# Optimization experiments

Hardware: AMD Instinct MI355X
Metric: run time of the kernel (lower is better)

## Reference

```python
import jax, jax.numpy as jnp
import numpy as np

N = 100_000      # nodes
E = 1_600_000    # edges (before self-loops)
IN_DIM = 128
HID = 64
NEG_SLOPE = 0.2  # PyG GATConv default


def gat_layer(x, src, dst, W, att_src, att_dst, bias, heads, out_ch):
    """PyG-style GATConv: messages flow src -> dst, softmax over incoming edges of dst."""
    n = x.shape[0]
    h = (x @ W).reshape(n, heads, out_ch)                 # [N,H,C]
    a_src = jnp.einsum('nhc,hc->nh', h, att_src)          # [N,H]
    a_dst = jnp.einsum('nhc,hc->nh', h, att_dst)          # [N,H]
    e = jax.nn.leaky_relu(a_src[src] + a_dst[dst], NEG_SLOPE)  # [E,H]
    # segment softmax over edges grouped by destination node
    m = jax.ops.segment_max(e, dst, num_segments=n)       # [N,H]
    ex = jnp.exp(e - m[dst])                              # [E,H]
    denom = jax.ops.segment_sum(ex, dst, num_segments=n)  # [N,H]
    alpha = ex / denom[dst]                               # [E,H]
    msg = alpha[:, :, None] * h[src]                      # [E,H,C]
    out = jax.ops.segment_sum(msg, dst, num_segments=n)   # [N,H,C]
    return out.reshape(n, heads * out_ch) + bias


def setup_inputs() -> dict:
    key = jax.random.key(0)
    ks = jax.random.split(key, 12)
    s = 0.1
    x = jax.random.normal(ks[0], (N, IN_DIM), jnp.float32)
    edge_index = jax.random.randint(ks[1], (2, E), 0, N, dtype=jnp.int32)
    # conv1: in_dim -> hidden, heads=2 (concat)
    W1 = jax.random.normal(ks[2], (IN_DIM, 2 * HID), jnp.float32) * s
    att_src1 = jax.random.normal(ks[3], (2, HID), jnp.float32) * s
    att_dst1 = jax.random.normal(ks[4], (2, HID), jnp.float32) * s
    b1 = jnp.zeros((2 * HID,), jnp.float32)
    # conv2: 2*hidden -> 1, heads=1
    W2 = jax.random.normal(ks[5], (2 * HID, 1), jnp.float32) * s
    att_src2 = jax.random.normal(ks[6], (1, 1), jnp.float32) * s
    att_dst2 = jax.random.normal(ks[7], (1, 1), jnp.float32) * s
    b2 = jnp.zeros((1,), jnp.float32)
    return {"x": x, "edge_index": edge_index,
            "W1": W1, "att_src1": att_src1, "att_dst1": att_dst1, "b1": b1,
            "W2": W2, "att_src2": att_src2, "att_dst2": att_dst2, "b2": b2}


def reference(x, edge_index, W1, att_src1, att_dst1, b1, W2, att_src2, att_dst2, b2):
    n = x.shape[0]
    # PyG GATConv default: add self-loops
    loop = jnp.arange(n, dtype=edge_index.dtype)
    src = jnp.concatenate([edge_index[0], loop])
    dst = jnp.concatenate([edge_index[1], loop])
    h = jax.nn.relu(gat_layer(x, src, dst, W1, att_src1, att_dst1, b1, heads=2, out_ch=HID))
    out = gat_layer(h, src, dst, W2, att_src2, att_dst2, b2, heads=1, out_ch=1)
    return jax.nn.sigmoid(out)  # [N,1]
```

## Files before the change

### kernel.cpp

```cpp
#include <hip/hip_runtime.h>
#include <hip/hip_bf16.h>
#include <hip/hip_fp8.h>
#include <hip/hip_fp16.h>

#define NEG 0.2f
#define CAP 48
#define TILE 8192
typedef unsigned int u32;
typedef unsigned short u16;
typedef unsigned char u8;
typedef unsigned long long u64;
typedef __attribute__((ext_vector_type(8))) short s8v;
typedef __attribute__((ext_vector_type(4))) float f4v;
typedef __attribute__((ext_vector_type(2))) float f2v;

__global__ __launch_bounds__(256) void binA_k(const int* __restrict__ ei,
                                              int2* __restrict__ meta,
                                              u64* __restrict__ slabs,
                                              int E, int Etot, int NB, int ntiles){
  __shared__ int bcnt[512], sc[512], bcur[512];
  int tile = blockIdx.x, tid = threadIdx.x;
  int base = tile*TILE;
  int cnt = min(TILE, Etot - base);
  for (int i=tid;i<512;i+=256) bcnt[i]=0;
  __syncthreads();
  for (int i=tid;i<cnt;i+=256){
    int e = base+i;
    int d = (e<E)? ei[E+e] : e-E;
    atomicAdd(&bcnt[d>>8], 1);
  }
  __syncthreads();
  for (int i=tid;i<512;i+=256) sc[i]=bcnt[i];
  __syncthreads();
  for (int o=1;o<512;o<<=1){
    int i0=tid, i1=tid+256;
    int r0 = (i0>=o)? sc[i0-o]:0;
    int r1 = (i1>=o)? sc[i1-o]:0;
    __syncthreads();
    sc[i0]+=r0; sc[i1]+=r1;
    __syncthreads();
  }
  for (int i=tid;i<512;i+=256) bcur[i] = sc[i]-bcnt[i];
  __syncthreads();
  for (int b=tid;b<NB;b+=256)
    meta[(size_t)b*ntiles + tile] = make_int2(sc[b]-bcnt[b], bcnt[b]);
  for (int i=tid;i<cnt;i+=256){
    int e = base+i;
    int d = (e<E)? ei[E+e] : e-E;
    int s = (e<E)? ei[e]   : d;
    int p = atomicAdd(&bcur[d>>8], 1);
    slabs[(size_t)base + p] = ((u64)(u32)d << 32) | (u32)s;
  }
}

__global__ __launch_bounds__(256) void binB_k(const u64* __restrict__ slabs,
                                              const int2* __restrict__ meta,
                                              const float2* __restrict__ as1,
                                              const float2* __restrict__ ad1,
                                              int* __restrict__ cur,
                                              u64* __restrict__ combo,
                                              float2* __restrict__ den,
                                              int N, int ntiles){
  int b = blockIdx.x, tid = threadIdx.x;
  int lo = b<<8;
  int nn = min(256, N-lo);
  __shared__ int lcur[256];
  __shared__ float sden0[256], sden1[256];
  __shared__ float2 sad[256];
  lcur[tid]=0; sden0[tid]=0.f; sden1[tid]=0.f;
  sad[tid] = (tid<nn)? ad1[lo+tid] : make_float2(0.f,0.f);
  __syncthreads();
  int grp = tid>>4, l16 = tid&15;
  const int2* mrow = meta + (size_t)b*ntiles;
  for (int t=grp; t<ntiles; t+=16){
    int2 m = mrow[t];
    const u64* sp = slabs + (size_t)t*TILE + m.x;
    for (int i=l16; i<m.y; i+=16){
      u64 pk = sp[i];
      int d = (int)(pk>>32), s = (int)(u32)pk;
      int dl = d & 255;
      float2 av = as1[s];
      float2 adv = sad[dl];
      float e0 = av.x+adv.x; e0 = (e0>0.f)? e0 : NEG*e0;
      float e1 = av.y+adv.y; e1 = (e1>0.f)? e1 : NEG*e1;
      __half2 hw = __floats2half2_rn(__expf(e0), __expf(e1));
      float2 wr = __half22float2(hw);
      atomicAdd(&sden0[dl], wr.x);
      atomicAdd(&sden1[dl], wr.y);
      int p = atomicAdd(&lcur[dl], 1);
      u32 wb = *(u32*)&hw;
      if (p < CAP) combo[(size_t)p*N + d] = ((u64)wb << 32) | (u32)s;
    }
  }
  __syncthreads();
  if (tid < nn){
    cur[lo+tid] = lcur[tid];
    den[lo+tid] = make_float2(sden0[tid], sden1[tid]);
  }
}

__global__ __launch_bounds__(256) void wt_k(const float* __restrict__ W, u16* __restrict__ Wt){
  int g = blockIdx.x*256 + threadIdx.x;
  int k = g >> 7, c = g & 127;
  __hip_bfloat16 b = __float2bfloat16(W[g]);
  Wt[c*128 + k] = *(u16*)&b;
}

__global__ __launch_bounds__(256) void gemm_k(const float* __restrict__ x,
                                              const u16* __restrict__ Wt,
                                              const float* __restrict__ aw_s,
                                              const float* __restrict__ aw_d,
                                              u8*  __restrict__ h1f,
                                              float2* __restrict__ as1,
                                              float2* __restrict__ ad1, int N){
  __shared__ u16 xs[128*136];
  __shared__ u16 ws[128*136];
  int tid = threadIdx.x;
  int rowBase = blockIdx.x * 128;
  #pragma unroll
  for (int i=0;i<16;i++){
    int j = i*256 + tid;
    int c = j >> 5, k4 = j & 31;
    *(uint2*)&ws[c*136 + k4*4] = ((const uint2*)Wt)[j];
  }
  #pragma unroll
  for (int i=0;i<16;i++){
    int j = i*256 + tid;
    int r = j >> 5, c4 = j & 31;
    float4 v = make_float4(0.f,0.f,0.f,0.f);
    if (rowBase + r < N) v = ((const float4*)x)[(size_t)(rowBase+r)*32 + c4];
    __hip_bfloat16 b0=__float2bfloat16(v.x), b1=__float2bfloat16(v.y);
    __hip_bfloat16 b2=__float2bfloat16(v.z), b3=__float2bfloat16(v.w);
    u32 w0 = (u32)*(u16*)&b0 | ((u32)*(u16*)&b1 << 16);
    u32 w1 = (u32)*(u16*)&b2 | ((u32)*(u16*)&b3 << 16);
    *(uint2*)&xs[r*136 + c4*4] = make_uint2(w0, w1);
  }
  __syncthreads();
  int wv = tid >> 6, lane = tid & 63;
  int lr = lane & 15, lk = lane >> 4;
  f4v acc[2][8];
  #pragma unroll
  for (int rt=0;rt<2;rt++)
    #pragma unroll
    for (int ct=0;ct<8;ct++) acc[rt][ct] = (f4v){0.f,0.f,0.f,0.f};
  #pragma unroll
  for (int ks=0; ks<4; ks++){
    int koff = ks*32 + lk*8;
    s8v bfrag[8];
    #pragma unroll
    for (int ct=0; ct<8; ct++)
      bfrag[ct] = *(s8v*)&ws[(ct*16 + lr)*136 + koff];
    #pragma unroll
    for (int rt=0; rt<2; rt++){
      int row = wv*32 + rt*16 + lr;
      s8v afrag = *(s8v*)&xs[row*136 + koff];
      #pragma unroll
      for (int ct=0; ct<8; ct++)
        acc[rt][ct] = __builtin_amdgcn_mfma_f32_16x16x32_bf16(afrag, bfrag[ct], acc[rt][ct], 0,0,0);
    }
  }
  #pragma unroll
  for (int rt=0; rt<2; rt++){
    float lps0[4]={0,0,0,0}, lps1[4]={0,0,0,0}, lpd0[4]={0,0,0,0}, lpd1[4]={0,0,0,0};
    int nodeB = rowBase + wv*32 + rt*16 + lk*4;
    #pragma unroll
    for (int ct=0; ct<8; ct++){
      int ch = ct*16 + lr;
      float aws = aw_s[ch], awd = aw_d[ch];
      #pragma unroll
      for (int reg=0; reg<4; reg++){
        float v = acc[rt][ct][reg];
        if (ct < 4){ lps0[reg] = fmaf(v, aws, lps0[reg]); lpd0[reg] = fmaf(v, awd, lpd0[reg]); }
        else       { lps1[reg] = fmaf(v, aws, lps1[reg]); lpd1[reg] = fmaf(v, awd, lpd1[reg]); }
      }
      int pk01 = __builtin_amdgcn_cvt_pk_fp8_f32(acc[rt][ct][0], acc[rt][ct][1], 0, false);
      int pk23 = __builtin_amdgcn_cvt_pk_fp8_f32(acc[rt][ct][2], acc[rt][ct][3], 0, false);
      if (nodeB + 0 < N) h1f[(size_t)(nodeB+0)*128 + ch] = (u8)(pk01 & 0xff);
      if (nodeB + 1 < N) h1f[(size_t)(nodeB+1)*128 + ch] = (u8)((pk01 >> 8) & 0xff);
      if (nodeB + 2 < N) h1f[(size_t)(nodeB+2)*128 + ch] = (u8)(pk23 & 0xff);
      if (nodeB + 3 < N) h1f[(size_t)(nodeB+3)*128 + ch] = (u8)((pk23 >> 8) & 0xff);
    }
    #pragma unroll
    for (int reg=0; reg<4; reg++){
      float a=lps0[reg], b=lps1[reg], c=lpd0[reg], d=lpd1[reg];
      #pragma unroll
      for (int o=1;o<16;o<<=1){
        a += __shfl_xor(a,o); b += __shfl_xor(b,o);
        c += __shfl_xor(c,o); d += __shfl_xor(d,o);
      }
      int node = nodeB + reg;
      if (lr == 0 && node < N){
        as1[node] = make_float2(a, b);
        ad1[node] = make_float2(c, d);
      }
    }
  }
}

__global__ __launch_bounds__(256) void agg1_k(const uint2* __restrict__ h1f2,
                                              const u64* __restrict__ combo,
                                              const float2* __restrict__ den,
                                              const int* __restrict__ cur,
                                              const float4* __restrict__ b1_4,
                                              const float4* __restrict__ W2_4,
                                              float* __restrict__ h2, int N){
  int w = threadIdx.x >> 6, l = threadIdx.x & 63;
  int g = l >> 4, li = l & 15;
  int n = blockIdx.x*16 + w*4 + g;
  if (n >= N) return;
  int deg = min(cur[n], CAP);
  bool hsel = (li >= 8);
  float2 dn = den[n];
  float rd = 1.f / (hsel ? dn.y : dn.x);
  float ac0=0.f,ac1=0.f,ac2=0.f,ac3=0.f,ac4=0.f,ac5=0.f,ac6=0.f,ac7=0.f;
  for (int kk = 0; kk < deg; kk += 8){
    u64 pk[8]; bool vd[8];
    #pragma unroll
    for (int j=0;j<8;j++){
      int idx = kk + j;
      vd[j] = idx < deg;
      pk[j] = combo[(size_t)(vd[j] ? idx : 0)*N + n];
    }
    uint2 hv[8];
    #pragma unroll
    for (int j=0;j<8;j++) hv[j] = h1f2[(size_t)(u32)(pk[j] & 0xffffffffu)*16 + li];
    #pragma unroll
    for (int j=0;j<8;j++){
      u32 wb = (u32)(pk[j] >> 32);
      __half2 hw = *(__half2*)&wb;
      float2 wf = __half22float2(hw);
      float gw = hsel ? wf.y : wf.x;
      gw = vd[j] ? gw : 0.f;
      f2v p0 = __builtin_amdgcn_cvt_pk_f32_fp8((int)hv[j].x, false);
      f2v p1 = __builtin_amdgcn_cvt_pk_f32_fp8((int)hv[j].x, true);
      f2v p2 = __builtin_amdgcn_cvt_pk_f32_fp8((int)hv[j].y, false);
      f2v p3 = __builtin_amdgcn_cvt_pk_f32_fp8((int)hv[j].y, true);
      ac0 = fmaf(gw, p0.x, ac0); ac1 = fmaf(gw, p0.y, ac1);
      ac2 = fmaf(gw, p1.x, ac2); ac3 = fmaf(gw, p1.y, ac3);
      ac4 = fmaf(gw, p2.x, ac4); ac5 = fmaf(gw, p2.y, ac5);
      ac6 = fmaf(gw, p3.x, ac6); ac7 = fmaf(gw, p3.y, ac7);
    }
  }
  float4 bb0 = b1_4[li*2], bb1 = b1_4[li*2+1];
  float4 ww0 = W2_4[li*2], ww1 = W2_4[li*2+1];
  float p = 0.f;
  p = fmaf(fmaxf(fmaf(ac0, rd, bb0.x), 0.f), ww0.x, p);
  p = fmaf(fmaxf(fmaf(ac1, rd, bb0.y), 0.f), ww0.y, p);
  p = fmaf(fmaxf(fmaf(ac2, rd, bb0.z), 0.f), ww0.z, p);
  p = fmaf(fmaxf(fmaf(ac3, rd, bb0.w), 0.f), ww0.w, p);
  p = fmaf(fmaxf(fmaf(ac4, rd, bb1.x), 0.f), ww1.x, p);
  p = fmaf(fmaxf(fmaf(ac5, rd, bb1.y), 0.f), ww1.y, p);
  p = fmaf(fmaxf(fmaf(ac6, rd, bb1.z), 0.f), ww1.z, p);
  p = fmaf(fmaxf(fmaf(ac7, rd, bb1.w), 0.f), ww1.w, p);
  #pragma unroll
  for (int o=1;o<16;o<<=1) p += __shfl_xor(p,o);
  if (li == 0) h2[n] = p;
}

__global__ __launch_bounds__(256) void agg2_k(const float* __restrict__ h2,
                                              const int* __restrict__ cur,
                                              const u64* __restrict__ combo,
                                              const float* __restrict__ att_s2,
                                              const float* __restrict__ att_d2,
                                              const float* __restrict__ b2,
                                              float* __restrict__ out, int N){
  int w = threadIdx.x >> 6, l = threadIdx.x & 63;
  int n = blockIdx.x*4 + w;
  if (n >= N) return;
  float as2 = att_s2[0], ad2 = att_d2[0];
  float hd = h2[n]*ad2;
  int deg = min(cur[n], CAP);
  bool v = l < deg;
  int s = (int)(u32)(combo[(size_t)(v ? l : 0)*N + n] & 0xffffffffu);
  float hs = h2[s];
  float e = fmaf(hs, as2, hd); e = (e>0.f)? e : NEG*e;
  float xv = v ? __expf(e) : 0.f;
  float den = xv, wsum = xv*hs;
  #pragma unroll
  for (int o=32;o>0;o>>=1){ den += __shfl_xor(den,o); wsum += __shfl_xor(wsum,o); }
  if (l == 0){
    float z = wsum/den + b2[0];
    out[n] = 1.f/(1.f + __expf(-z));
  }
}

extern "C" void kernel_launch(void* const* d_in, const int* in_sizes, int n_in,
                              void* d_out, int out_size, void* d_ws, size_t ws_size,
                              hipStream_t stream){
  const float* x     = (const float*)d_in[0];
  const int*   ei    = (const int*)d_in[1];
  const float* W1    = (const float*)d_in[2];
  const float* aw_s  = (const float*)d_in[3];
  const float* aw_d  = (const float*)d_in[4];
  const float* b1    = (const float*)d_in[5];
  const float* W2    = (const float*)d_in[6];
  const float* at_s2 = (const float*)d_in[7];
  const float* at_d2 = (const float*)d_in[8];
  const float* b2    = (const float*)d_in[9];
  float* out = (float*)d_out;

  const int N = in_sizes[0]/128;
  const int E = in_sizes[1]/2;
  const int Etot = E + N;
  const int ntiles = (Etot + TILE - 1) / TILE;
  const int NB = (N + 255) >> 8;

  auto align256 = [](size_t v){ return (v + 255) & ~(size_t)255; };
  char* w = (char*)d_ws;
  u8* h1f       = (u8*)w;     w += align256((size_t)N*128);
  float2* as1   = (float2*)w; w += align256((size_t)N*8);
  float2* ad1   = (float2*)w; w += align256((size_t)N*8);
  float* h2     = (float*)w;  w += align256((size_t)N*4);
  int* cur      = (int*)w;    w += align256((size_t)N*4);
  float2* den   = (float2*)w; w += align256((size_t)N*8);
  u16* Wt       = (u16*)w;    w += align256((size_t)128*128*2);
  u64* combo    = (u64*)w;    w += align256((size_t)N*CAP*8);
  u64* slabs    = (u64*)w;    w += align256((size_t)ntiles*TILE*8);
  int2* meta    = (int2*)w;   w += align256((size_t)NB*ntiles*8);

  const int tb = 256;
  binA_k<<<ntiles, tb, 0, stream>>>(ei, meta, slabs, E, Etot, NB, ntiles);
  wt_k<<<64, tb, 0, stream>>>(W1, Wt);
  gemm_k<<<(N+127)/128, tb, 0, stream>>>(x, Wt, aw_s, aw_d, h1f, as1, ad1, N);
  binB_k<<<NB, tb, 0, stream>>>(slabs, meta, as1, ad1, cur, combo, den, N, ntiles);
  agg1_k<<<(N+15)/16, tb, 0, stream>>>((const uint2*)h1f, combo, den, cur,
                                       (const float4*)b1, (const float4*)W2, h2, N);
  agg2_k<<<(N+3)/4, tb, 0, stream>>>(h2, cur, combo, at_s2, at_d2, b2, out, N);
}
```

Baseline: 172.0 us.

## Shrink binning tiles, cache edges in registers, prefetch tile metadata

```diff
diff --git a/kernel.cpp b/kernel.cpp
--- a/kernel.cpp
+++ b/kernel.cpp
@@ -5,7 +5,7 @@
 
 #define NEG 0.2f
 #define CAP 48
-#define TILE 8192
+#define TILE 2048
 typedef unsigned int u32;
 typedef unsigned short u16;
 typedef unsigned char u8;
@@ -24,13 +24,21 @@
   int cnt = min(TILE, Etot - base);
   for (int i=tid;i<512;i+=256) bcnt[i]=0;
   __syncthreads();
-  for (int i=tid;i<cnt;i+=256){
-    int e = base+i;
-    int d = (e<E)? ei[E+e] : e-E;
-    atomicAdd(&bcnt[d>>8], 1);
-  }
-  __syncthreads();
-  for (int i=tid;i<512;i+=256) sc[i]=bcnt[i];
+  int dd[8], ss[8];
+  #pragma unroll
+  for (int j=0;j<8;j++){
+    int i = tid + j*256;
+    if (i < cnt){
+      int e = base+i;
+      int d = (e<E)? ei[E+e] : e-E;
+      int s = (e<E)? ei[e]   : d;
+      dd[j] = d; ss[j] = s;
+      atomicAdd(&bcnt[d>>8], 1);
+    } else dd[j] = -1;
+  }
+  __syncthreads();
+  sc[tid]     = bcnt[tid];
+  sc[tid+256] = bcnt[tid+256];
   __syncthreads();
   for (int o=1;o<512;o<<=1){
     int i0=tid, i1=tid+256;
@@ -40,16 +48,17 @@
     sc[i0]+=r0; sc[i1]+=r1;
     __syncthreads();
   }
-  for (int i=tid;i<512;i+=256) bcur[i] = sc[i]-bcnt[i];
+  bcur[tid]     = sc[tid]     - bcnt[tid];
+  bcur[tid+256] = sc[tid+256] - bcnt[tid+256];
   __syncthreads();
   for (int b=tid;b<NB;b+=256)
     meta[(size_t)b*ntiles + tile] = make_int2(sc[b]-bcnt[b], bcnt[b]);
-  for (int i=tid;i<cnt;i+=256){
-    int e = base+i;
-    int d = (e<E)? ei[E+e] : e-E;
-    int s = (e<E)? ei[e]   : d;
-    int p = atomicAdd(&bcur[d>>8], 1);
-    slabs[(size_t)base + p] = ((u64)(u32)d << 32) | (u32)s;
+  #pragma unroll
+  for (int j=0;j<8;j++){
+    if (dd[j] >= 0){
+      int p = atomicAdd(&bcur[dd[j]>>8], 1);
+      slabs[(size_t)base + p] = ((u64)(u32)dd[j] << 32) | (u32)ss[j];
+    }
   }
 }
 
@@ -70,12 +79,13 @@
   lcur[tid]=0; sden0[tid]=0.f; sden1[tid]=0.f;
   sad[tid] = (tid<nn)? ad1[lo+tid] : make_float2(0.f,0.f);
   __syncthreads();
-  int grp = tid>>4, l16 = tid&15;
+  int grp = tid>>3, l8 = tid&7;
   const int2* mrow = meta + (size_t)b*ntiles;
-  for (int t=grp; t<ntiles; t+=16){
-    int2 m = mrow[t];
+  int2 m = (grp < ntiles)? mrow[grp] : make_int2(0,0);
+  for (int t=grp; t<ntiles; t+=32){
+    int2 mn = (t+32 < ntiles)? mrow[t+32] : make_int2(0,0);
     const u64* sp = slabs + (size_t)t*TILE + m.x;
-    for (int i=l16; i<m.y; i+=16){
+    for (int i=l8; i<m.y; i+=8){
       u64 pk = sp[i];
       int d = (int)(pk>>32), s = (int)(u32)pk;
       int dl = d & 255;
@@ -91,6 +101,7 @@
       u32 wb = *(u32*)&hw;
       if (p < CAP) combo[(size_t)p*N + d] = ((u64)wb << 32) | (u32)s;
     }
+    m = mn;
   }
   __syncthreads();
   if (tid < nn){
```

After: 171.1 us. Within noise of the previous version (-0.5%).
